# Kernel tuning notes

Measured on AMD Instinct MI355X. Metric: run time of the kernel, lower is better.

Reference implementation:

```python
import jax, jax.numpy as jnp
import numpy as np

# ---- config (matches init_kwargs) ----
D_MODEL = 1024
D_STATE = 16
D_CONV = 4
EXPAND = 2
HEADDIM = 32
NGROUPS = 1
CHUNK = 256
D_INNER = EXPAND * D_MODEL            # 2048
NHEADS = D_INNER // HEADDIM           # 64
D_IN_PROJ = 2 * D_INNER + 2 * NGROUPS * D_STATE + NHEADS  # 4176
CONV_DIM = D_INNER + 2 * NGROUPS * D_STATE                # 2080
BATCH, SEQLEN = 2, 2048
EPS = 1e-5
NEG_INF = -1e9


def setup_inputs() -> dict:
    key = jax.random.key(0)
    ks = jax.random.split(key, 8)
    u = jax.random.normal(ks[0], (BATCH, SEQLEN, D_MODEL), jnp.float32)
    W_in = jax.random.normal(ks[1], (D_IN_PROJ, D_MODEL), jnp.float32) * (1.0 / np.sqrt(D_MODEL))
    conv_w = jax.random.normal(ks[2], (CONV_DIM, 1, D_CONV), jnp.float32) * (1.0 / np.sqrt(D_CONV))
    conv_b = jnp.zeros((CONV_DIM,), jnp.float32)
    dt_bias = jax.random.normal(ks[3], (NHEADS,), jnp.float32) * 0.1
    A_log = jnp.log(1.0 + 15.0 * jax.random.uniform(ks[4], (NHEADS,), jnp.float32))  # A in [1,16]
    D = jnp.ones((NHEADS,), jnp.float32)
    norm_w = jnp.ones((D_INNER,), jnp.float32)
    W_out = jax.random.normal(ks[5], (D_MODEL, D_INNER), jnp.float32) * (1.0 / np.sqrt(D_INNER))
    return dict(u=u, W_in=W_in, conv_w=conv_w, conv_b=conv_b, dt_bias=dt_bias,
                A_log=A_log, D=D, norm_w=norm_w, W_out=W_out)


def _ssd_chunk_scan(x, dt, A, Bm, Cm, Dh):
    """Mamba2 SSD chunked scan.
    x: (b,l,h,p), dt: (b,l,h), A: (h,), Bm/Cm: (b,l,n) [ngroups=1], Dh: (h,).
    """
    b, l, h, p = x.shape
    c = l // CHUNK
    n = Bm.shape[-1]
    xdt = x * dt[..., None]                                  # (b,l,h,p)
    xc = xdt.reshape(b, c, CHUNK, h, p)
    xo = x.reshape(b, c, CHUNK, h, p)
    Bc = Bm.reshape(b, c, CHUNK, n)
    Cc = Cm.reshape(b, c, CHUNK, n)
    Abar = (dt * A).reshape(b, c, CHUNK, h).transpose(0, 3, 1, 2)   # (b,h,c,l)
    Acum = jnp.cumsum(Abar, axis=-1)                                # (b,h,c,l)
    # intra-chunk decay matrix L[i,j] = exp(sum_{j<k<=i} Abar_k), causal
    seg = Acum[..., :, None] - Acum[..., None, :]                   # (b,h,c,l,l)
    causal = jnp.tril(jnp.ones((CHUNK, CHUNK), bool))
    Lmat = jnp.exp(jnp.where(causal, seg, NEG_INF))
    # diagonal (intra-chunk) contribution
    Yd = jnp.einsum('bcln,bcsn,bhcls,bcshp->bclhp', Cc, Bc, Lmat, xc)
    # chunk states
    decay_states = jnp.exp(Acum[..., -1:] - Acum)                   # (b,h,c,l)
    states = jnp.einsum('bcln,bhcl,bclhp->bchpn', Bc, decay_states, xc)
    chunk_decay = jnp.exp(Acum[..., -1])                            # (b,h,c)
    # inter-chunk recurrence over the c axis
    def step(carry, inp):
        s, dec = inp
        new = dec[..., None, None] * carry + s
        return new, carry
    s_t = jnp.moveaxis(states, 1, 0)            # (c,b,h,p,n)
    d_t = jnp.moveaxis(chunk_decay, -1, 0)      # (c,b,h)
    init = jnp.zeros((b, h, p, n), x.dtype)
    _, prev = jax.lax.scan(step, init, (s_t, d_t))
    prev = jnp.moveaxis(prev, 0, 1)             # (b,c,h,p,n) state entering each chunk
    Yo = jnp.einsum('bcln,bchpn,bhcl->bclhp', Cc, prev, jnp.exp(Acum))
    Y = Yd + Yo + xo * Dh[None, None, None, :, None]
    return Y.reshape(b, l, h, p)


def reference(u, W_in, conv_w, conv_b, dt_bias, A_log, D, norm_w, W_out):
    b, l, _ = u.shape
    zxbcdt = u @ W_in.T                                   # (b,l,D_IN_PROJ)
    z = zxbcdt[..., :D_INNER]
    xBC = zxbcdt[..., D_INNER:D_INNER + CONV_DIM]
    dt = jax.nn.softplus(zxbcdt[..., -NHEADS:] + dt_bias)  # (b,l,h)
    # depthwise causal conv1d + SiLU
    xBC_t = xBC.transpose(0, 2, 1)                        # (b, CONV_DIM, l)
    conv = jax.lax.conv_general_dilated(
        xBC_t, conv_w, window_strides=(1,), padding=[(D_CONV - 1, 0)],
        feature_group_count=CONV_DIM)
    xBC = jax.nn.silu(conv + conv_b[None, :, None]).transpose(0, 2, 1)
    x = xBC[..., :D_INNER]
    Bm = xBC[..., D_INNER:D_INNER + NGROUPS * D_STATE]
    Cm = xBC[..., D_INNER + NGROUPS * D_STATE:]
    A = -jnp.exp(A_log)
    Y = _ssd_chunk_scan(x.reshape(b, l, NHEADS, HEADDIM), dt, A, Bm, Cm, D)
    y = Y.reshape(b, l, D_INNER)
    # gated RMSNorm (norm_before_gate=False): normalize(y * silu(z)) * w
    yg = y * jax.nn.silu(z)
    yn = yg * jax.lax.rsqrt(jnp.mean(yg * yg, axis=-1, keepdims=True) + EPS) * norm_w
    out = yn @ W_out.T
    return (out, z)
```

## Files before the change

### kernel.cpp

```cpp
#include <hip/hip_runtime.h>

#define BATCH   2
#define SEQLEN  2048
#define DMODEL  1024
#define DINNER  2048
#define NHEADS  64
#define HEADDIM 32
#define DSTATE  16
#define CONVDIM 2080
#define DINPROJ 4192
#define NPAD    4224
#define CHUNK   256
#define NCHUNK  8
#define BL      (BATCH*SEQLEN)
#define XWIDTH  2144

typedef float  f4    __attribute__((ext_vector_type(4)));
typedef short  s16x8 __attribute__((ext_vector_type(8)));
typedef __bf16 bf16x8 __attribute__((ext_vector_type(8)));
typedef float  f32x4v __attribute__((ext_vector_type(4)));

#define MFMA16(a,b,c) __builtin_amdgcn_mfma_f32_16x16x32_bf16((a),(b),(c),0,0,0)

__device__ __forceinline__ unsigned short f2bf(float f){
  unsigned int u = __float_as_uint(f);
  u += 0x7FFFu + ((u >> 16) & 1u);
  return (unsigned short)(u >> 16);
}

__device__ __forceinline__ void gload_lds16(const void* g, void* l){
  __builtin_amdgcn_global_load_lds((const __attribute__((address_space(1))) unsigned int*)g,
                                   (__attribute__((address_space(3))) unsigned int*)l,
                                   16, 0, 0);
}

__device__ __forceinline__ bf16x8 f32x8_to_frag(const float* src, bool valid){
  bf16x8 r;
  if (valid) {
    f4 a = *(const f4*)src;
    f4 c = *(const f4*)(src + 4);
    r[0]=(__bf16)a[0]; r[1]=(__bf16)a[1]; r[2]=(__bf16)a[2]; r[3]=(__bf16)a[3];
    r[4]=(__bf16)c[0]; r[5]=(__bf16)c[1]; r[6]=(__bf16)c[2]; r[7]=(__bf16)c[3];
  } else {
    r[0]=(__bf16)0.f; r[1]=(__bf16)0.f; r[2]=(__bf16)0.f; r[3]=(__bf16)0.f;
    r[4]=(__bf16)0.f; r[5]=(__bf16)0.f; r[6]=(__bf16)0.f; r[7]=(__bf16)0.f;
  }
  return r;
}

__global__ void cast_f32_bf16(const float* __restrict__ in, unsigned short* __restrict__ out, int n){
  int i = blockIdx.x * 256 + threadIdx.x;
  if (i < n) out[i] = f2bf(in[i]);
}

__global__ void cast_win_pad(const float* __restrict__ in, unsigned short* __restrict__ out){
  int i = blockIdx.x * 256 + threadIdx.x;
  if (i >= NPAD * DMODEL) return;
  int r = i >> 10;
  out[i] = (r < DINPROJ) ? f2bf(in[i]) : (unsigned short)0;
}

template<int MODE>
__global__ __launch_bounds__(256) void gemm_bf16(
    const unsigned short* __restrict__ A,
    const unsigned short* __restrict__ B,
    int K, float* __restrict__ C0, float* __restrict__ C1, int N)
{
  __shared__ unsigned short As[128][32];
  __shared__ unsigned short Bs[128][32];
  const int tid  = threadIdx.x;
  const int bm   = blockIdx.y, bn = blockIdx.x;
  const int wave = tid >> 6, lane = tid & 63;
  const int wm   = (wave >> 1) * 64, wn = (wave & 1) * 64;
  const int lrow = lane & 15, lko = (lane >> 4) * 8;

  const int srow = wave * 16 + (lane >> 2);
  const int scol = (lane & 3) * 8;
  const unsigned short* Ag = A + (size_t)(bm * 128 + srow) * K + scol;
  const unsigned short* Bg = B + (size_t)(bn * 128 + srow) * K + scol;
  unsigned short* As0 = &As[wave * 16][0];
  unsigned short* As1 = &As[64 + wave * 16][0];
  unsigned short* Bs0 = &Bs[wave * 16][0];
  unsigned short* Bs1 = &Bs[64 + wave * 16][0];

  f32x4v acc[4][4];
  #pragma unroll
  for (int i = 0; i < 4; ++i)
    #pragma unroll
    for (int j = 0; j < 4; ++j)
      acc[i][j] = (f32x4v){0.f,0.f,0.f,0.f};

  for (int k0 = 0; k0 < K; k0 += 32) {
    gload_lds16(Ag, As0);
    gload_lds16(Ag + (size_t)64 * K, As1);
    gload_lds16(Bg, Bs0);
    gload_lds16(Bg + (size_t)64 * K, Bs1);
    __syncthreads();
    bf16x8 af[4], bfr[4];
    #pragma unroll
    for (int i = 0; i < 4; ++i) {
      af[i]  = *(const bf16x8*)&As[wm + i * 16 + lrow][lko];
      bfr[i] = *(const bf16x8*)&Bs[wn + i * 16 + lrow][lko];
    }
    #pragma unroll
    for (int mi = 0; mi < 4; ++mi)
      #pragma unroll
      for (int ni = 0; ni < 4; ++ni)
        acc[mi][ni] = MFMA16(af[mi], bfr[ni], acc[mi][ni]);
    __syncthreads();
    Ag += 32; Bg += 32;
  }

  const int orow0 = bm * 128 + wm;
  const int ocol0 = bn * 128 + wn;
  #pragma unroll
  for (int mi = 0; mi < 4; ++mi)
    #pragma unroll
    for (int ni = 0; ni < 4; ++ni) {
      int col  = ocol0 + ni * 16 + (lane & 15);
      int rowb = orow0 + mi * 16 + (lane >> 4) * 4;
      #pragma unroll
      for (int r = 0; r < 4; ++r) {
        int row = rowb + r;
        float v = acc[mi][ni][r];
        if (MODE == 0) {
          if (col < DINNER)        C0[(size_t)row * DINNER + col] = v;
          else if (col < DINPROJ)  C1[(size_t)row * XWIDTH + (col - DINNER)] = v;
        } else {
          C0[(size_t)row * N + col] = v;
        }
      }
    }
}

__global__ void conv_dt_kernel(const float* __restrict__ xbcdt,
                               const float* __restrict__ conv_w, const float* __restrict__ conv_b,
                               const float* __restrict__ dt_bias,
                               float* __restrict__ xconv, float* __restrict__ dtout)
{
  int idx = blockIdx.x * 256 + threadIdx.x;
  if (idx >= BL * XWIDTH) return;
  int ch = idx % XWIDTH;
  int bl = idx / XWIDTH;
  int l  = bl & (SEQLEN - 1);
  if (ch < CONVDIM) {
    float acc = conv_b[ch];
    #pragma unroll
    for (int j = 0; j < 4; ++j) {
      int ls = l - 3 + j;
      float x = (ls >= 0) ? xbcdt[(size_t)(bl - 3 + j) * XWIDTH + ch] : 0.f;
      acc += conv_w[ch * 4 + j] * x;
    }
    float s = acc / (1.f + __expf(-acc));
    xconv[(size_t)bl * CONVDIM + ch] = s;
  } else {
    int h = ch - CONVDIM;
    float x = xbcdt[(size_t)bl * XWIDTH + ch] + dt_bias[h];
    float dtv = (x > 20.f) ? x : log1pf(__expf(x));
    dtout[bl * NHEADS + h] = dtv;
  }
}

__global__ __launch_bounds__(256) void ssd_phaseA(
    const float* __restrict__ xconv, const float* __restrict__ dt,
    const float* __restrict__ A_log,
    float* __restrict__ acum, float* __restrict__ decay, float* __restrict__ states)
{
  int bc = blockIdx.x, h = blockIdx.y;
  int b = bc >> 3;
  int t = threadIdx.x;
  __shared__ float sAc[256], sCoef[256], sDt[256];
  __shared__ float sB[256][16];
  __shared__ float sX[256][32];
  int rowbase = b * SEQLEN + (bc & 7) * CHUNK;
  float dtv = dt[(rowbase + t) * NHEADS + h];
  float Av  = -__expf(A_log[h]);
  sAc[t] = dtv * Av; sDt[t] = dtv;
  for (int i = t; i < 256 * 16; i += 256) { int l = i >> 4, n = i & 15; sB[l][n] = xconv[(size_t)(rowbase + l) * CONVDIM + DINNER + n]; }
  for (int i = t; i < 256 * 32; i += 256) { int l = i >> 5, p = i & 31; sX[l][p] = xconv[(size_t)(rowbase + l) * CONVDIM + h * 32 + p]; }
  __syncthreads();
  for (int off = 1; off < 256; off <<= 1) {
    float add = (t >= off) ? sAc[t - off] : 0.f;
    __syncthreads();
    sAc[t] += add;
    __syncthreads();
  }
  int bch = bc * 64 + h;
  acum[(size_t)bch * 256 + t] = sAc[t];
  float last = sAc[255];
  if (t == 0) decay[bch] = __expf(last);
  sCoef[t] = sDt[t] * __expf(last - sAc[t]);
  __syncthreads();
  #pragma unroll
  for (int o = 0; o < 2; ++o) {
    int oi = t + o * 256;
    int p = oi >> 4, n = oi & 15;
    float acc = 0.f;
    for (int l = 0; l < 256; ++l) acc += sCoef[l] * sB[l][n] * sX[l][p];
    states[(size_t)bch * 512 + oi] = acc;
  }
}

__global__ void ssd_phaseB(const float* __restrict__ states, const float* __restrict__ decay,
                           float* __restrict__ prev)
{
  int bh = blockIdx.x;
  int b = bh >> 6, h = bh & 63;
  int t = threadIdx.x;
  float carry = 0.f;
  for (int c = 0; c < NCHUNK; ++c) {
    int bch = (b * 8 + c) * 64 + h;
    size_t base = (size_t)bch * 512 + t;
    prev[base] = carry;
    carry = decay[bch] * carry + states[base];
  }
}

__global__ __launch_bounds__(256, 2) void ssd_phaseC_mfma(
    const float* __restrict__ xconv, const float* __restrict__ dt,
    const float* __restrict__ acum, const float* __restrict__ prev,
    const float* __restrict__ Dvec, float* __restrict__ y)
{
  const int bc = blockIdx.x, h = blockIdx.y;
  const int b = bc >> 3;
  const int rowbase = b * SEQLEN + (bc & 7) * CHUNK;
  const int bch = bc * 64 + h;
  const int tid = threadIdx.x, wave = tid >> 6, lane = tid & 63;
  const int l16 = lane & 15, khalf = lane >> 4;

  __shared__ float sAcum[256];
  __shared__ __bf16 sXT[32][264];
  __shared__ __bf16 sP[4][2][16][40];

  if (tid < 256) sAcum[tid] = acum[(size_t)bch * 256 + tid];
  {
    int l  = tid >> 3;
    int p0 = (tid & 7) * 4;
    #pragma unroll
    for (int pass = 0; pass < 8; ++pass) {
      int ls = l + pass * 32;
      const float* xr = xconv + (size_t)(rowbase + ls) * CONVDIM + h * 32 + p0;
      f4 v = *(const f4*)xr;
      float dtl = dt[(rowbase + ls) * NHEADS + h];
      #pragma unroll
      for (int j = 0; j < 4; ++j) sXT[p0 + j][ls] = (__bf16)(v[j] * dtl);
    }
  }

  const bool kv = (khalf < 2);
  bf16x8 bfr[16], cfr[4], pvf[2];
  #pragma unroll
  for (int i = 0; i < 16; ++i)
    bfr[i] = f32x8_to_frag(xconv + (size_t)(rowbase + i * 16 + l16) * CONVDIM + DINNER + khalf * 8, kv);
  #pragma unroll
  for (int t = 0; t < 4; ++t)
    cfr[t] = f32x8_to_frag(xconv + (size_t)(rowbase + (wave + 4 * t) * 16 + l16) * CONVDIM + DINNER + DSTATE + khalf * 8, kv);
  #pragma unroll
  for (int pt = 0; pt < 2; ++pt)
    pvf[pt] = f32x8_to_frag(prev + (size_t)bch * 512 + (pt * 16 + l16) * 16 + khalf * 8, kv);
  __syncthreads();

  const float Dh = Dvec[h];
  #pragma unroll
  for (int t = 0; t < 4; ++t) {
    const int LT = wave + 4 * t;
    const int lbase = LT * 16;
    float al[4], el[4];
    #pragma unroll
    for (int r = 0; r < 4; ++r) { al[r] = sAcum[lbase + khalf * 4 + r]; el[r] = __expf(al[r]); }
    f32x4v y0 = MFMA16(cfr[t], pvf[0], ((f32x4v){0.f,0.f,0.f,0.f}));
    f32x4v y1 = MFMA16(cfr[t], pvf[1], ((f32x4v){0.f,0.f,0.f,0.f}));
    #pragma unroll
    for (int r = 0; r < 4; ++r) { y0[r] *= el[r]; y1[r] *= el[r]; }

    #pragma unroll
    for (int kp = 0; kp < 8; ++kp) {
      if (2 * kp <= LT) {
        f32x4v s0 = MFMA16(cfr[t], bfr[2 * kp],     ((f32x4v){0.f,0.f,0.f,0.f}));
        f32x4v s1 = MFMA16(cfr[t], bfr[2 * kp + 1], ((f32x4v){0.f,0.f,0.f,0.f}));
        const int buf = kp & 1;
        #pragma unroll
        for (int r = 0; r < 4; ++r) {
          int l  = lbase + khalf * 4 + r;
          int sA = 2 * kp * 16 + l16;
          int sB2 = sA + 16;
          float p0 = (sA  <= l) ? s0[r] * __expf(al[r] - sAcum[sA])  : 0.f;
          float p1 = (sB2 <= l) ? s1[r] * __expf(al[r] - sAcum[sB2]) : 0.f;
          sP[wave][buf][khalf * 4 + r][l16]      = (__bf16)p0;
          sP[wave][buf][khalf * 4 + r][16 + l16] = (__bf16)p1;
        }
        bf16x8 pa  = *(const bf16x8*)&sP[wave][buf][l16][khalf * 8];
        bf16x8 xf0 = *(const bf16x8*)&sXT[l16][kp * 32 + khalf * 8];
        bf16x8 xf1 = *(const bf16x8*)&sXT[16 + l16][kp * 32 + khalf * 8];
        y0 = MFMA16(pa, xf0, y0);
        y1 = MFMA16(pa, xf1, y1);
      }
    }

    #pragma unroll
    for (int r = 0; r < 4; ++r) {
      int lg = rowbase + lbase + khalf * 4 + r;
      const float* xr = xconv + (size_t)lg * CONVDIM + h * 32;
      float* yr = y + (size_t)lg * DINNER + h * 32;
      yr[l16]      = y0[r] + Dh * xr[l16];
      yr[16 + l16] = y1[r] + Dh * xr[16 + l16];
    }
  }
}

__global__ __launch_bounds__(256) void gate_norm(const float* __restrict__ y,
    const float* __restrict__ z, const float* __restrict__ norm_w,
    unsigned short* __restrict__ ynbf)
{
  int row = blockIdx.x, t = threadIdx.x;
  const float* yr = y + (size_t)row * DINNER;
  const float* zr = z + (size_t)row * DINNER;
  float vals[8];
  float ss = 0.f;
  #pragma unroll
  for (int i = 0; i < 8; ++i) {
    int ci = t + i * 256;
    float zv = zr[ci];
    float g = zv / (1.f + __expf(-zv));
    float v = yr[ci] * g;
    vals[i] = v; ss += v * v;
  }
  #pragma unroll
  for (int o = 1; o < 64; o <<= 1) ss += __shfl_xor(ss, o);
  __shared__ float sred[4];
  if ((t & 63) == 0) sred[t >> 6] = ss;
  __syncthreads();
  float tot = sred[0] + sred[1] + sred[2] + sred[3];
  float scale = rsqrtf(tot * (1.f / DINNER) + 1e-5f);
  #pragma unroll
  for (int i = 0; i < 8; ++i) {
    int ci = t + i * 256;
    ynbf[(size_t)row * DINNER + ci] = f2bf(vals[i] * scale * norm_w[ci]);
  }
}

extern "C" void kernel_launch(void* const* d_in, const int* in_sizes, int n_in,
                              void* d_out, int out_size, void* d_ws, size_t ws_size,
                              hipStream_t stream)
{
  const float* u       = (const float*)d_in[0];
  const float* W_in    = (const float*)d_in[1];
  const float* conv_w  = (const float*)d_in[2];
  const float* conv_b  = (const float*)d_in[3];
  const float* dt_bias = (const float*)d_in[4];
  const float* A_log   = (const float*)d_in[5];
  const float* Dv      = (const float*)d_in[6];
  const float* norm_w  = (const float*)d_in[7];
  const float* W_out   = (const float*)d_in[8];

  float* out  = (float*)d_out;
  float* zout = out + (size_t)BL * DMODEL;

  char* ws = (char*)d_ws;
  size_t off = 0;
  auto alloc = [&](size_t bytes){ size_t o = off; off += (bytes + 255) & ~(size_t)255; return o; };
  size_t o_ubf    = alloc((size_t)BL * DMODEL * 2);
  size_t o_wbf    = alloc((size_t)NPAD * DMODEL * 2);
  size_t o_xbcdt  = alloc((size_t)BL * XWIDTH * 4);
  size_t o_xconv  = alloc((size_t)BL * CONVDIM * 4);
  size_t o_dt     = alloc((size_t)BL * NHEADS * 4);
  size_t o_acum   = alloc((size_t)1024 * 256 * 4);
  size_t o_decay  = alloc((size_t)1024 * 4);
  size_t o_states = alloc((size_t)1024 * 512 * 4);
  size_t o_prev   = alloc((size_t)1024 * 512 * 4);
  size_t o_ynbf   = alloc((size_t)BL * DINNER * 2);

  unsigned short* ubf    = (unsigned short*)(ws + o_ubf);
  unsigned short* wbf    = (unsigned short*)(ws + o_wbf);
  float*          xbcdt  = (float*)(ws + o_xbcdt);
  float*          xconv  = (float*)(ws + o_xconv);
  float*          dtws   = (float*)(ws + o_dt);
  float*          acum   = (float*)(ws + o_acum);
  float*          decay  = (float*)(ws + o_decay);
  float*          states = (float*)(ws + o_states);
  float*          prevb  = (float*)(ws + o_prev);
  unsigned short* ynbf   = (unsigned short*)(ws + o_ynbf);
  unsigned short* woutbf = ubf;
  float*          ywork  = xbcdt;

  cast_f32_bf16<<<(BL * DMODEL) / 256, 256, 0, stream>>>(u, ubf, BL * DMODEL);
  cast_win_pad<<<(NPAD * DMODEL) / 256, 256, 0, stream>>>(W_in, wbf);

  gemm_bf16<0><<<dim3(NPAD / 128, BL / 128), 256, 0, stream>>>(ubf, wbf, DMODEL, zout, xbcdt, 0);

  conv_dt_kernel<<<(BL * XWIDTH) / 256, 256, 0, stream>>>(xbcdt, conv_w, conv_b, dt_bias, xconv, dtws);

  ssd_phaseA<<<dim3(16, 64), 256, 0, stream>>>(xconv, dtws, A_log, acum, decay, states);
  ssd_phaseB<<<128, 512, 0, stream>>>(states, decay, prevb);
  ssd_phaseC_mfma<<<dim3(16, 64), 256, 0, stream>>>(xconv, dtws, acum, prevb, Dv, ywork);

  gate_norm<<<BL, 256, 0, stream>>>(ywork, zout, norm_w, ynbf);

  cast_f32_bf16<<<(DMODEL * DINNER) / 256, 256, 0, stream>>>(W_out, woutbf, DMODEL * DINNER);

  gemm_bf16<1><<<dim3(DMODEL / 128, BL / 128), 256, 0, stream>>>(ynbf, woutbf, DINNER, out, nullptr, DMODEL);
}
```

Measured before the change: 256.4 us.

## Double-buffer GEMM LDS tiles, swizzle LDS columns, and remap block order

Loads the next K-tile into a second shared-memory buffer while MFMAs run on the current one, dropping one barrier per iteration. It also XOR-swizzles the LDS column layout to reduce bank conflicts on fragment reads, and remaps block indices in groups of eight to change the cache locality of tiles. This doubles LDS usage and assumes the grid size divides evenly by 8. The async global-to-LDS loads may also need explicit waits to stay correct.

```diff
diff --git a/kernel.cpp b/kernel.cpp
--- a/kernel.cpp
+++ b/kernel.cpp
@@ -66,22 +66,26 @@
     const unsigned short* __restrict__ B,
     int K, float* __restrict__ C0, float* __restrict__ C1, int N)
 {
-  __shared__ unsigned short As[128][32];
-  __shared__ unsigned short Bs[128][32];
+  __shared__ unsigned short As[2][128][32];
+  __shared__ unsigned short Bs[2][128][32];
+
+  const int nx   = gridDim.x;
+  const int flat = blockIdx.y * nx + blockIdx.x;
+  const int q    = (nx * gridDim.y) >> 3;
+  const int swz  = (flat & 7) * q + (flat >> 3);
+  const int bm   = swz / nx, bn = swz % nx;
+
   const int tid  = threadIdx.x;
-  const int bm   = blockIdx.y, bn = blockIdx.x;
   const int wave = tid >> 6, lane = tid & 63;
   const int wm   = (wave >> 1) * 64, wn = (wave & 1) * 64;
-  const int lrow = lane & 15, lko = (lane >> 4) * 8;
+  const int lrow = lane & 15, khalf = lane >> 4;
+  const int cswz = (khalf ^ (lrow & 3)) * 8;
 
   const int srow = wave * 16 + (lane >> 2);
-  const int scol = (lane & 3) * 8;
+  const int scol = (((lane & 3) ^ ((lane >> 2) & 3))) * 8;
   const unsigned short* Ag = A + (size_t)(bm * 128 + srow) * K + scol;
   const unsigned short* Bg = B + (size_t)(bn * 128 + srow) * K + scol;
-  unsigned short* As0 = &As[wave * 16][0];
-  unsigned short* As1 = &As[64 + wave * 16][0];
-  unsigned short* Bs0 = &Bs[wave * 16][0];
-  unsigned short* Bs1 = &Bs[64 + wave * 16][0];
+  const int lr0 = wave * 16;
 
   f32x4v acc[4][4];
   #pragma unroll
@@ -90,25 +94,31 @@
     for (int j = 0; j < 4; ++j)
       acc[i][j] = (f32x4v){0.f,0.f,0.f,0.f};
 
-  for (int k0 = 0; k0 < K; k0 += 32) {
-    gload_lds16(Ag, As0);
-    gload_lds16(Ag + (size_t)64 * K, As1);
-    gload_lds16(Bg, Bs0);
-    gload_lds16(Bg + (size_t)64 * K, Bs1);
-    __syncthreads();
+  auto stage = [&](int buf, int k0){
+    gload_lds16(Ag + k0,                   &As[buf][lr0][0]);
+    gload_lds16(Ag + k0 + (size_t)64 * K,  &As[buf][64 + lr0][0]);
+    gload_lds16(Bg + k0,                   &Bs[buf][lr0][0]);
+    gload_lds16(Bg + k0 + (size_t)64 * K,  &Bs[buf][64 + lr0][0]);
+  };
+
+  const int NT = K >> 5;
+  stage(0, 0);
+  __syncthreads();
+  for (int t = 0; t < NT; ++t) {
+    const int cur = t & 1;
+    if (t + 1 < NT) stage(cur ^ 1, (t + 1) << 5);
     bf16x8 af[4], bfr[4];
     #pragma unroll
     for (int i = 0; i < 4; ++i) {
-      af[i]  = *(const bf16x8*)&As[wm + i * 16 + lrow][lko];
-      bfr[i] = *(const bf16x8*)&Bs[wn + i * 16 + lrow][lko];
+      af[i]  = *(const bf16x8*)&As[cur][wm + i * 16 + lrow][cswz];
+      bfr[i] = *(const bf16x8*)&Bs[cur][wn + i * 16 + lrow][cswz];
     }
     #pragma unroll
     for (int mi = 0; mi < 4; ++mi)
       #pragma unroll
       for (int ni = 0; ni < 4; ++ni)
         acc[mi][ni] = MFMA16(af[mi], bfr[ni], acc[mi][ni]);
-    __syncthreads();
-    Ag += 32; Bg += 32;
+    if (t + 1 < NT) __syncthreads();
   }
 
   const int orow0 = bm * 128 + wm;
```

Measured after the change: 246.3 us. 3.9% less time.
